# Optimization experiments

Hardware: AMD Instinct MI355X
Metric: run time of the kernel (lower is better)

The kernel has to match this reference:

```python
import jax, jax.numpy as jnp
import numpy as np

N = 100000   # nodes
E = 1600000  # edges
NC = 10000   # candidates
G = 1000     # graphs
ND = 32      # node_emb_dim
ED = 8       # edge_emb_dim
L = 4        # num_layers


def setup_inputs() -> dict:
    key = jax.random.key(0)
    ks = jax.random.split(key, 12)
    s = 0.1
    return {
        "x": jax.random.normal(ks[0], (N, 2), dtype=jnp.float32),
        "edge_attr": jax.random.normal(ks[1], (E, 1), dtype=jnp.float32),
        "Wn_in": jax.random.normal(ks[2], (2, ND)) * s,
        "bn_in": jnp.zeros((ND,)),
        "We_in": jax.random.normal(ks[3], (1, ED)) * s,
        "be_in": jnp.zeros((ED,)),
        "We_l": jax.random.normal(ks[4], (L, 2 * ND + ED, ED)) * s,
        "be_l": jnp.zeros((L, ED)),
        "Wn_l": jax.random.normal(ks[5], (L, ND + ED, ND)) * s,
        "bn_l": jnp.zeros((L, ND)),
        "Wout": jax.random.normal(ks[6], (ND, 1)) * s,
        "bout": jnp.zeros((1,)),
        "edge_index": jax.random.randint(ks[7], (2, E), 0, N),
        "batch": jnp.sort(jax.random.randint(ks[8], (N,), 0, G)),
        "candidate_idxs": jax.random.randint(ks[9], (NC,), 0, N),
    }


def reference(x, edge_attr, Wn_in, bn_in, We_in, be_in, We_l, be_l, Wn_l, bn_l,
              Wout, bout, edge_index, batch, candidate_idxs):
    h = x @ Wn_in + bn_in            # [N, ND]
    e = edge_attr @ We_in + be_in    # [E, ED]
    src, dst = edge_index[0], edge_index[1]
    for l in range(L):
        # edge update: MLP on [x_src, x_dst, edge_attr]
        m = jnp.concatenate([h[src], h[dst], e], axis=-1)        # [E, 2*ND+ED]
        new_e = jax.nn.relu(m @ We_l[l] + be_l[l])               # [E, ED]
        # aggregate (aggr='add') messages at destination nodes
        agg = jax.ops.segment_sum(new_e, dst, num_segments=N)    # [N, ED]
        new_h = jax.nn.relu(jnp.concatenate([h, agg], axis=-1) @ Wn_l[l] + bn_l[l])
        h = h + new_h   # residual
        e = e + new_e   # residual
    logits = (h[candidate_idxs] @ Wout + bout)[:, 0]             # [NC]
    seg = batch[candidate_idxs]                                  # [NC] graph ids
    # scatter_log_softmax over per-graph candidate groups
    mx = jax.ops.segment_max(logits, seg, num_segments=G)
    shifted = logits - mx[seg]
    lse = jnp.log(jax.ops.segment_sum(jnp.exp(shifted), seg, num_segments=G))
    return shifted - lse[seg]
```

## Files before the change

kernel.cpp:

```cpp
#include <hip/hip_runtime.h>

#define ND 32
#define ED 8
#define NL 4
#define NG 1000
#define NBC_MAX 512
#define CHUNK 8192
#define CHUNK_H 4096
#define NBLK 64

typedef unsigned short u16;

__device__ __forceinline__ int xcd_swizzle(int b, int nb) {
  int per = nb >> 3;
  return (b < (per << 3)) ? ((b & 7) * per + (b >> 3)) : b;
}


__device__ __forceinline__ u16 f2bf(float f) {
  unsigned u = __float_as_uint(f);
  u += 0x7fffu + ((u >> 16) & 1u);
  return (u16)(u >> 16);
}
__device__ __forceinline__ unsigned pack2(float a, float b) {
  return (unsigned)f2bf(a) | ((unsigned)f2bf(b) << 16);
}
__device__ __forceinline__ void cvt8(uint4 p, float* o) {
  o[0] = __uint_as_float(p.x << 16); o[1] = __uint_as_float(p.x & 0xffff0000u);
  o[2] = __uint_as_float(p.y << 16); o[3] = __uint_as_float(p.y & 0xffff0000u);
  o[4] = __uint_as_float(p.z << 16); o[5] = __uint_as_float(p.z & 0xffff0000u);
  o[6] = __uint_as_float(p.w << 16); o[7] = __uint_as_float(p.w & 0xffff0000u);
}
__device__ __forceinline__ uint4 pack8(const float* v) {
  uint4 o;
  o.x = pack2(v[0], v[1]); o.y = pack2(v[2], v[3]);
  o.z = pack2(v[4], v[5]); o.w = pack2(v[6], v[7]);
  return o;
}


__global__ void k_init_h(const float* __restrict__ x,
                         const float* __restrict__ W,
                         const float* __restrict__ b,
                         const float* __restrict__ We,
                         const float* __restrict__ be,
                         u16* __restrict__ h,
                         u16* __restrict__ zs, u16* __restrict__ zd,
                         int N) {
  int n = xcd_swizzle(blockIdx.x, gridDim.x) * blockDim.x + threadIdx.x;
  if (n >= N) return;
  float x0 = x[2 * n], x1 = x[2 * n + 1];
  float v[ND];
#pragma unroll
  for (int d = 0; d < ND; ++d) v[d] = fmaf(x0, W[d], fmaf(x1, W[ND + d], b[d]));
#pragma unroll
  for (int d = 0; d < ND; ++d) v[d] = __uint_as_float((unsigned)f2bf(v[d]) << 16);
  uint4* h4 = reinterpret_cast<uint4*>(h + (size_t)n * ND);
#pragma unroll
  for (int q = 0; q < 4; ++q) h4[q] = pack8(&v[q * 8]);
  float zsv[ED], zdv[ED];
#pragma unroll
  for (int j = 0; j < ED; ++j) { zsv[j] = 0.0f; zdv[j] = be[j]; }
#pragma unroll
  for (int k = 0; k < ND; ++k)
#pragma unroll
    for (int j = 0; j < ED; ++j) {
      zsv[j] = fmaf(v[k], We[k * ED + j], zsv[j]);
      zdv[j] = fmaf(v[k], We[(ND + k) * ED + j], zdv[j]);
    }
  *reinterpret_cast<uint4*>(zs + (size_t)n * ED) = pack8(zsv);
  *reinterpret_cast<uint4*>(zd + (size_t)n * ED) = pack8(zdv);
}


__global__ void k_chist(const int* __restrict__ dst, int* __restrict__ bcnt,
                        int E, int nbc) {
  __shared__ int lcnt[NBC_MAX];
  for (int b = threadIdx.x; b < nbc; b += blockDim.x) lcnt[b] = 0;
  __syncthreads();
  int e0 = blockIdx.x * CHUNK_H;
  int e1 = min(e0 + CHUNK_H, E);
  for (int i = e0 + threadIdx.x; i < e1; i += blockDim.x)
    atomicAdd(&lcnt[dst[i] >> 8], 1);
  __syncthreads();
  for (int b = threadIdx.x; b < nbc; b += blockDim.x)
    if (lcnt[b]) atomicAdd(&bcnt[b], lcnt[b]);
}

__global__ void k_cscan(const int* __restrict__ bcnt, int* __restrict__ bbase,
                        int nbc) {
  __shared__ int s[NBC_MAX];
  int tid = threadIdx.x;
  if (nbc <= NBC_MAX) {
    int v = (tid < nbc) ? bcnt[tid] : 0;
    s[tid] = v;
    __syncthreads();
    for (int st = 1; st < NBC_MAX; st <<= 1) {
      int t = (tid >= st) ? s[tid - st] : 0;
      __syncthreads();
      s[tid] += t;
      __syncthreads();
    }
    if (tid < nbc) bbase[tid] = s[tid] - v;
    if (tid == nbc - 1) bbase[nbc] = s[tid];
  } else if (tid == 0) {
    int run = 0;
    for (int i = 0; i < nbc; ++i) { bbase[i] = run; run += bcnt[i]; }
    bbase[nbc] = run;
  }
}

__global__ void k_binA(const int* __restrict__ src, const int* __restrict__ dst,
                       const float* __restrict__ ea,
                       const int* __restrict__ bbase, int* __restrict__ cursor_c,
                       uint2* __restrict__ binned, int E, int nbc) {
  __shared__ int lcnt[NBC_MAX];
  __shared__ int lbase[NBC_MAX];
  for (int b = threadIdx.x; b < nbc; b += blockDim.x) lcnt[b] = 0;
  __syncthreads();
  int e0 = blockIdx.x * CHUNK;
  int e1 = min(e0 + CHUNK, E);
  for (int i = e0 + threadIdx.x; i < e1; i += blockDim.x)
    atomicAdd(&lcnt[dst[i] >> 8], 1);
  __syncthreads();
  for (int b = threadIdx.x; b < nbc; b += blockDim.x) {
    int c = lcnt[b];
    lbase[b] = c ? (bbase[b] + atomicAdd(&cursor_c[b], c)) : 0;
  }
  __syncthreads();
  for (int i = e0 + threadIdx.x; i < e1; i += blockDim.x) {
    int d = dst[i];
    int pos = atomicAdd(&lbase[d >> 8], 1);
    binned[pos] = make_uint2((unsigned)src[i] | ((unsigned)(d & 255) << 24),
                             __float_as_uint(ea[i]));
  }
}

__global__ void k_binB(const uint2* __restrict__ binned,
                       const int* __restrict__ bbase,
                       int* __restrict__ ssrc, float* __restrict__ ea_s,
                       int* __restrict__ noffs,
                       int N) {
  __shared__ int hist[256];
  __shared__ int scn[256];
  int b = blockIdx.x;
  int base = bbase[b], end = bbase[b + 1];
  int node0 = b << 8;
  int nn = min(256, N - node0);
  hist[threadIdx.x] = 0;
  __syncthreads();
  for (int p = base + threadIdx.x; p < end; p += blockDim.x)
    atomicAdd(&hist[binned[p].x >> 24], 1);
  __syncthreads();
  int v = hist[threadIdx.x];
  scn[threadIdx.x] = v;
  __syncthreads();
  for (int st = 1; st < 256; st <<= 1) {
    int t = (threadIdx.x >= (unsigned)st) ? scn[threadIdx.x - st] : 0;
    __syncthreads();
    scn[threadIdx.x] += t;
    __syncthreads();
  }
  int excl = base + scn[threadIdx.x] - v;
  if ((int)threadIdx.x < nn) noffs[node0 + threadIdx.x] = excl;
  if (threadIdx.x == 0) noffs[min(node0 + 256, N)] = end;
  hist[threadIdx.x] = excl;
  __syncthreads();
  for (int p = base + threadIdx.x; p < end; p += blockDim.x) {
    uint2 rec = binned[p];
    int dl = (int)(rec.x >> 24);
    int pos = atomicAdd(&hist[dl], 1);
    ssrc[pos] = (int)(rec.x & 0xffffffu);
    ea_s[pos] = __uint_as_float(rec.y);
  }
}

template <int L0>
__global__ void k_layer(u16* __restrict__ h,
                        u16* __restrict__ e,
                        const float* __restrict__ ea_s,
                        const int* __restrict__ ssrc,
                        const int* __restrict__ noffs,
                        const u16* __restrict__ zs,
                        const u16* __restrict__ zd,
                        const float* __restrict__ Wei,
                        const float* __restrict__ bei,
                        const float* __restrict__ W3,
                        const float* __restrict__ Wn,
                        const float* __restrict__ bn,
                        const float* __restrict__ Wen,
                        const float* __restrict__ ben,
                        u16* __restrict__ zs_n, u16* __restrict__ zd_n,
                        int N) {
  int t = xcd_swizzle(blockIdx.x, gridDim.x) * blockDim.x + threadIdx.x;
  int n = t >> 2;
  int g = t & 3;
  if (n >= N) return;
  int o0 = noffs[n], o1 = noffs[n + 1];
  float zdv[ED];
  cvt8(*reinterpret_cast<const uint4*>(zd + (size_t)n * ED), zdv);
  float av[ED];
#pragma unroll
  for (int j = 0; j < ED; ++j) av[j] = 0.0f;
  for (int p = o0 + g; p < o1; p += 4) {
    int s = ssrc[p];
    float zsv[ED];
    cvt8(*reinterpret_cast<const uint4*>(zs + (size_t)s * ED), zsv);
    float ein[ED];
    if (L0) {
      float a = ea_s[p];
#pragma unroll
      for (int j = 0; j < ED; ++j) ein[j] = fmaf(a, Wei[j], bei[j]);
    } else {
      cvt8(*reinterpret_cast<const uint4*>(e + (size_t)p * ED), ein);
    }
    float acc[ED];
#pragma unroll
    for (int j = 0; j < ED; ++j) acc[j] = zsv[j] + zdv[j];
#pragma unroll
    for (int k = 0; k < ED; ++k)
#pragma unroll
      for (int j = 0; j < ED; ++j)
        acc[j] = fmaf(ein[k], W3[k * ED + j], acc[j]);
    float eo[ED];
#pragma unroll
    for (int j = 0; j < ED; ++j) {
      float r = fmaxf(acc[j], 0.0f);
      av[j] += r;
      eo[j] = ein[j] + r;
    }
    *reinterpret_cast<uint4*>(e + (size_t)p * ED) = pack8(eo);
  }
#pragma unroll
  for (int j = 0; j < ED; ++j) {
    av[j] += __shfl_xor(av[j], 1);
    av[j] += __shfl_xor(av[j], 2);
  }
  uint4* h4 = reinterpret_cast<uint4*>(h + (size_t)n * ND);
  float hv[ND];
#pragma unroll
  for (int q = 0; q < 4; ++q) cvt8(h4[q], &hv[q * 8]);
  const int j0 = g * 8;
  float acc8[8];
#pragma unroll
  for (int jj = 0; jj < 8; ++jj) acc8[jj] = bn[j0 + jj];
#pragma unroll
  for (int k = 0; k < ND; ++k)
#pragma unroll
    for (int jj = 0; jj < 8; ++jj)
      acc8[jj] = fmaf(hv[k], Wn[k * ND + j0 + jj], acc8[jj]);
#pragma unroll
  for (int k = 0; k < ED; ++k)
#pragma unroll
    for (int jj = 0; jj < 8; ++jj)
      acc8[jj] = fmaf(av[k], Wn[(ND + k) * ND + j0 + jj], acc8[jj]);
  float hn8[8];
#pragma unroll
  for (int jj = 0; jj < 8; ++jj) {
    float o = hv[j0 + jj] + fmaxf(acc8[jj], 0.0f);
    hn8[jj] = __uint_as_float((unsigned)f2bf(o) << 16);
  }
  h4[g] = pack8(hn8);
  float pz[2 * ED];
#pragma unroll
  for (int j = 0; j < 2 * ED; ++j) pz[j] = 0.0f;
#pragma unroll
  for (int kk = 0; kk < 8; ++kk) {
    float hk = hn8[kk];
    int krow = j0 + kk;
#pragma unroll
    for (int j = 0; j < ED; ++j) {
      pz[j] = fmaf(hk, Wen[krow * ED + j], pz[j]);
      pz[ED + j] = fmaf(hk, Wen[(ND + krow) * ED + j], pz[ED + j]);
    }
  }
#pragma unroll
  for (int j = 0; j < 2 * ED; ++j) {
    pz[j] += __shfl_xor(pz[j], 1);
    pz[j] += __shfl_xor(pz[j], 2);
  }
  if (g == 0) {
    *reinterpret_cast<uint4*>(zs_n + (size_t)n * ED) = pack8(pz);
  } else if (g == 1) {
    float zdo[ED];
#pragma unroll
    for (int j = 0; j < ED; ++j) zdo[j] = pz[ED + j] + ben[j];
    *reinterpret_cast<uint4*>(zd_n + (size_t)n * ED) = pack8(zdo);
  }
}


__device__ __forceinline__ unsigned int enc_f32(float f) {
  unsigned int bits = __float_as_uint(f);
  return (bits & 0x80000000u) ? ~bits : (bits | 0x80000000u);
}
__device__ __forceinline__ float dec_f32(unsigned int u) {
  unsigned int bits = (u & 0x80000000u) ? (u ^ 0x80000000u) : ~u;
  return __uint_as_float(bits);
}

__global__ void k_cand(const u16* __restrict__ h,
                       const u16* __restrict__ e,
                       const u16* __restrict__ zs,
                       const u16* __restrict__ zd,
                       const int* __restrict__ ssrc,
                       const int* __restrict__ noffs,
                       const int* __restrict__ cand,
                       const int* __restrict__ batch,
                       const float* __restrict__ W3,
                       const float* __restrict__ Wn,
                       const float* __restrict__ bn,
                       const float* __restrict__ Wout,
                       const float* __restrict__ bout,
                       float* __restrict__ logits,
                       int* __restrict__ seg,
                       unsigned int* __restrict__ mxu,
                       int NC) {
  int t = blockIdx.x * blockDim.x + threadIdx.x;
  int c = t >> 3, g = t & 7;
  if (c >= NC) return;
  int n = cand[c];
  int o0 = noffs[n], o1 = noffs[n + 1];
  float zdv[ED];
  cvt8(*reinterpret_cast<const uint4*>(zd + (size_t)n * ED), zdv);
  float av[ED];
#pragma unroll
  for (int j = 0; j < ED; ++j) av[j] = 0.0f;
  for (int p = o0 + g; p < o1; p += 8) {
    int s = ssrc[p];
    float zsv[ED], ein[ED], acc[ED];
    cvt8(*reinterpret_cast<const uint4*>(zs + (size_t)s * ED), zsv);
    cvt8(*reinterpret_cast<const uint4*>(e + (size_t)p * ED), ein);
#pragma unroll
    for (int j = 0; j < ED; ++j) acc[j] = zsv[j] + zdv[j];
#pragma unroll
    for (int k = 0; k < ED; ++k)
#pragma unroll
      for (int j = 0; j < ED; ++j)
        acc[j] = fmaf(ein[k], W3[k * ED + j], acc[j]);
#pragma unroll
    for (int j = 0; j < ED; ++j) av[j] += fmaxf(acc[j], 0.0f);
  }
#pragma unroll
  for (int j = 0; j < ED; ++j) {
    av[j] += __shfl_xor(av[j], 1);
    av[j] += __shfl_xor(av[j], 2);
    av[j] += __shfl_xor(av[j], 4);
  }
  const uint4* h4 = reinterpret_cast<const uint4*>(h + (size_t)n * ND);
  float hv[ND];
#pragma unroll
  for (int q = 0; q < 4; ++q) cvt8(h4[q], &hv[q * 8]);
  const int j0 = g * 4;
  float acc4[4];
#pragma unroll
  for (int jj = 0; jj < 4; ++jj) acc4[jj] = bn[j0 + jj];
#pragma unroll
  for (int k = 0; k < ND; ++k)
#pragma unroll
    for (int jj = 0; jj < 4; ++jj)
      acc4[jj] = fmaf(hv[k], Wn[k * ND + j0 + jj], acc4[jj]);
#pragma unroll
  for (int k = 0; k < ED; ++k)
#pragma unroll
    for (int jj = 0; jj < 4; ++jj)
      acc4[jj] = fmaf(av[k], Wn[(ND + k) * ND + j0 + jj], acc4[jj]);
  float lg = 0.0f;
#pragma unroll
  for (int jj = 0; jj < 4; ++jj)
    lg = fmaf(hv[j0 + jj] + fmaxf(acc4[jj], 0.0f), Wout[j0 + jj], lg);
  lg += __shfl_xor(lg, 1);
  lg += __shfl_xor(lg, 2);
  lg += __shfl_xor(lg, 4);
  if (g == 0) {
    lg += bout[0];
    logits[c] = lg;
    int gr = batch[n];
    seg[c] = gr;
    atomicMax(&mxu[gr], enc_f32(lg));
  }
}

__global__ void k_expsum(float* __restrict__ logits,
                         const int* __restrict__ seg,
                         const unsigned int* __restrict__ mxu,
                         float* __restrict__ sum,
                         int NC) {
  int c = blockIdx.x * blockDim.x + threadIdx.x;
  if (c >= NC) return;
  int g = seg[c];
  float sh = logits[c] - dec_f32(mxu[g]);
  logits[c] = sh;
  atomicAdd(&sum[g], expf(sh));
}

__global__ void k_final(const float* __restrict__ shifted,
                        const int* __restrict__ seg,
                        const float* __restrict__ sum,
                        float* __restrict__ out, int NC) {
  int c = blockIdx.x * blockDim.x + threadIdx.x;
  if (c >= NC) return;
  out[c] = shifted[c] - logf(sum[seg[c]]);
}


extern "C" void kernel_launch(void* const* d_in, const int* in_sizes, int n_in,
                              void* d_out, int out_size, void* d_ws, size_t ws_size,
                              hipStream_t stream) {
  const float* x       = (const float*)d_in[0];
  const float* ea      = (const float*)d_in[1];
  const float* Wn_in   = (const float*)d_in[2];
  const float* bn_in   = (const float*)d_in[3];
  const float* We_in   = (const float*)d_in[4];
  const float* be_in   = (const float*)d_in[5];
  const float* We_l    = (const float*)d_in[6];
  const float* be_l    = (const float*)d_in[7];
  const float* Wn_l    = (const float*)d_in[8];
  const float* bn_l    = (const float*)d_in[9];
  const float* Wout    = (const float*)d_in[10];
  const float* bout    = (const float*)d_in[11];
  const int* edge_index= (const int*)d_in[12];
  const int* batch     = (const int*)d_in[13];
  const int* cand      = (const int*)d_in[14];

  const int N  = in_sizes[13];
  const int E  = in_sizes[1];
  const int NC = in_sizes[14];
  const int nbc = (N + 255) >> 8;

  char* ws = (char*)d_ws;
  uint2* binned = (uint2*)ws; ws += (size_t)E * sizeof(uint2);
  int*   ssrc   = (int*)ws;   ws += (size_t)E * sizeof(int);
  float* ea_s   = (float*)ws; ws += (size_t)E * sizeof(float);
  u16*   h      = (u16*)ws;   ws += (size_t)N * ND * sizeof(u16);
  u16*   e      = (u16*)ws;   ws += (size_t)E * ED * sizeof(u16);
  u16*   zs0    = (u16*)ws;   ws += (size_t)N * ED * sizeof(u16);
  u16*   zd0    = (u16*)ws;   ws += (size_t)N * ED * sizeof(u16);
  u16*   zs1    = (u16*)ws;   ws += (size_t)N * ED * sizeof(u16);
  u16*   zd1    = (u16*)ws;   ws += (size_t)N * ED * sizeof(u16);
  int*   noffs  = (int*)ws;   ws += ((size_t)N + 4) * sizeof(int);
  int*   bcnt   = (int*)ws;   ws += (size_t)NBC_MAX * sizeof(int);
  int*   cursor = (int*)ws;   ws += (size_t)NBC_MAX * sizeof(int);
  int*   bbase  = (int*)ws;   ws += ((size_t)NBC_MAX + 4) * sizeof(int);
  float* logits = (float*)ws; ws += (size_t)NC * sizeof(float);
  int*   seg    = (int*)ws;   ws += (size_t)NC * sizeof(int);
  unsigned int* mxu = (unsigned int*)ws; ws += (size_t)NG * sizeof(unsigned int);
  float* sum    = (float*)ws; ws += (size_t)NG * sizeof(float);

  const int* srcp = edge_index;
  const int* dstp = edge_index + E;
  const int blk = 256;
  const size_t WE_STRIDE = (size_t)(2 * ND + ED) * ED;

  hipMemsetAsync(bcnt, 0, 2 * (size_t)NBC_MAX * sizeof(int), stream);
  k_chist<<<(E + CHUNK_H - 1) / CHUNK_H, 1024, 0, stream>>>(dstp, bcnt, E, nbc);
  k_cscan<<<1, NBC_MAX, 0, stream>>>(bcnt, bbase, nbc);
  k_binA<<<(E + CHUNK - 1) / CHUNK, 1024, 0, stream>>>(srcp, dstp, ea, bbase,
                                                       cursor, binned, E, nbc);
  k_binB<<<nbc, 256, 0, stream>>>(binned, bbase, ssrc, ea_s, noffs, N);

  k_init_h<<<(N + NBLK - 1) / NBLK, NBLK, 0, stream>>>(x, Wn_in, bn_in, We_l,
                                                       be_l, h, zs0, zd0, N);

  const int ngrid4 = (N + 63) / 64;
  u16* zsc = zs0; u16* zdc = zd0;
  u16* zsn = zs1; u16* zdn = zd1;
  for (int l = 0; l < NL - 1; ++l) {
    const float* W3 = We_l + l * WE_STRIDE + (size_t)2 * ND * ED;
    const float* Wn = Wn_l + (size_t)l * (ND + ED) * ND;
    const float* bn = bn_l + (size_t)l * ND;
    const float* Wen = We_l + (l + 1) * WE_STRIDE;
    const float* ben = be_l + (size_t)(l + 1) * ED;
    if (l == 0) {
      k_layer<1><<<ngrid4, 256, 0, stream>>>(
          h, e, ea_s, ssrc, noffs, zsc, zdc, We_in, be_in, W3, Wn, bn,
          Wen, ben, zsn, zdn, N);
    } else {
      k_layer<0><<<ngrid4, 256, 0, stream>>>(
          h, e, ea_s, ssrc, noffs, zsc, zdc, We_in, be_in, W3, Wn, bn,
          Wen, ben, zsn, zdn, N);
    }
    u16* t;
    t = zsc; zsc = zsn; zsn = t;
    t = zdc; zdc = zdn; zdn = t;
  }

  hipMemsetAsync(mxu, 0, NG * (sizeof(unsigned int) + sizeof(float)), stream);
  {
    const int l = NL - 1;
    const float* W3 = We_l + l * WE_STRIDE + (size_t)2 * ND * ED;
    const float* Wn = Wn_l + (size_t)l * (ND + ED) * ND;
    const float* bn = bn_l + (size_t)l * ND;
    k_cand<<<((size_t)NC * 8 + 255) / 256, 256, 0, stream>>>(
        h, e, zsc, zdc, ssrc, noffs, cand, batch, W3, Wn, bn, Wout, bout,
        logits, seg, mxu, NC);
  }
  k_expsum<<<(NC + blk - 1) / blk, blk, 0, stream>>>(logits, seg, mxu, sum, NC);
  k_final<<<(NC + blk - 1) / blk, blk, 0, stream>>>(logits, seg, sum,
                                                    (float*)d_out, NC);
}
```

Measured before the change: 372.2 us.

## Use 8 lanes per node and software-prefetch edge gathers in layer kernels

The layer kernel now assigns 8 threads per node instead of 4, so each thread walks every eighth edge and computes 4 of the 32 node outputs, with an extra shuffle stage for the reductions. Both the layer and candidate kernels gain a two-deep software pipeline: the next edge's source index and edge data are loaded ahead, and the dependent zs gather is issued one iteration early. The aim is to hide the latency of the indirect gathers and expose more parallelism per node. In exchange, register pressure goes up and lanes are wasted on low-degree nodes.

```diff
diff --git a/kernel.cpp b/kernel.cpp
--- a/kernel.cpp
+++ b/kernel.cpp
@@ -193,28 +193,50 @@
                         u16* __restrict__ zs_n, u16* __restrict__ zd_n,
                         int N) {
   int t = xcd_swizzle(blockIdx.x, gridDim.x) * blockDim.x + threadIdx.x;
-  int n = t >> 2;
-  int g = t & 3;
+  int n = t >> 3;
+  int g = t & 7;
   if (n >= N) return;
   int o0 = noffs[n], o1 = noffs[n + 1];
   float zdv[ED];
   cvt8(*reinterpret_cast<const uint4*>(zd + (size_t)n * ED), zdv);
+  const uint4* zs4 = reinterpret_cast<const uint4*>(zs);
+  const uint4* e4c = reinterpret_cast<const uint4*>(e);
+  uint4* e4 = reinterpret_cast<uint4*>(e);
   float av[ED];
 #pragma unroll
   for (int j = 0; j < ED; ++j) av[j] = 0.0f;
-  for (int p = o0 + g; p < o1; p += 4) {
-    int s = ssrc[p];
-    float zsv[ED];
-    cvt8(*reinterpret_cast<const uint4*>(zs + (size_t)s * ED), zsv);
-    float ein[ED];
+
+  int p = o0 + g;
+  int sA = 0, sB = 0;
+  uint4 eA = make_uint4(0, 0, 0, 0), eB = make_uint4(0, 0, 0, 0);
+  float aA = 0.0f, aB = 0.0f;
+  uint4 zA = make_uint4(0, 0, 0, 0);
+  if (p < o1) {
+    sA = ssrc[p];
+    if (L0) aA = ea_s[p]; else eA = e4c[p];
+    zA = zs4[sA];
+  }
+  if (p + 8 < o1) {
+    sB = ssrc[p + 8];
+    if (L0) aB = ea_s[p + 8]; else eB = e4c[p + 8];
+  }
+  for (; p < o1; ) {
+    int pn = p + 8, pc = p + 16;
+    uint4 zB = make_uint4(0, 0, 0, 0);
+    if (pn < o1) zB = zs4[sB];
+    int sC = 0; uint4 eC = make_uint4(0, 0, 0, 0); float aC = 0.0f;
+    if (pc < o1) {
+      sC = ssrc[pc];
+      if (L0) aC = ea_s[pc]; else eC = e4c[pc];
+    }
+    float zsv[ED], ein[ED], acc[ED];
+    cvt8(zA, zsv);
     if (L0) {
-      float a = ea_s[p];
-#pragma unroll
-      for (int j = 0; j < ED; ++j) ein[j] = fmaf(a, Wei[j], bei[j]);
+#pragma unroll
+      for (int j = 0; j < ED; ++j) ein[j] = fmaf(aA, Wei[j], bei[j]);
     } else {
-      cvt8(*reinterpret_cast<const uint4*>(e + (size_t)p * ED), ein);
-    }
-    float acc[ED];
+      cvt8(eA, ein);
+    }
 #pragma unroll
     for (int j = 0; j < ED; ++j) acc[j] = zsv[j] + zdv[j];
 #pragma unroll
@@ -229,44 +251,49 @@
       av[j] += r;
       eo[j] = ein[j] + r;
     }
-    *reinterpret_cast<uint4*>(e + (size_t)p * ED) = pack8(eo);
+    e4[p] = pack8(eo);
+    p = pn;
+    sA = sB; eA = eB; aA = aB; zA = zB;
+    sB = sC; eB = eC; aB = aC;
   }
 #pragma unroll
   for (int j = 0; j < ED; ++j) {
     av[j] += __shfl_xor(av[j], 1);
     av[j] += __shfl_xor(av[j], 2);
+    av[j] += __shfl_xor(av[j], 4);
   }
   uint4* h4 = reinterpret_cast<uint4*>(h + (size_t)n * ND);
   float hv[ND];
 #pragma unroll
   for (int q = 0; q < 4; ++q) cvt8(h4[q], &hv[q * 8]);
-  const int j0 = g * 8;
-  float acc8[8];
-#pragma unroll
-  for (int jj = 0; jj < 8; ++jj) acc8[jj] = bn[j0 + jj];
+  const int j0 = g * 4;
+  float acc4[4];
+#pragma unroll
+  for (int jj = 0; jj < 4; ++jj) acc4[jj] = bn[j0 + jj];
 #pragma unroll
   for (int k = 0; k < ND; ++k)
 #pragma unroll
-    for (int jj = 0; jj < 8; ++jj)
-      acc8[jj] = fmaf(hv[k], Wn[k * ND + j0 + jj], acc8[jj]);
+    for (int jj = 0; jj < 4; ++jj)
+      acc4[jj] = fmaf(hv[k], Wn[k * ND + j0 + jj], acc4[jj]);
 #pragma unroll
   for (int k = 0; k < ED; ++k)
 #pragma unroll
-    for (int jj = 0; jj < 8; ++jj)
-      acc8[jj] = fmaf(av[k], Wn[(ND + k) * ND + j0 + jj], acc8[jj]);
-  float hn8[8];
-#pragma unroll
-  for (int jj = 0; jj < 8; ++jj) {
-    float o = hv[j0 + jj] + fmaxf(acc8[jj], 0.0f);
-    hn8[jj] = __uint_as_float((unsigned)f2bf(o) << 16);
-  }
-  h4[g] = pack8(hn8);
+    for (int jj = 0; jj < 4; ++jj)
+      acc4[jj] = fmaf(av[k], Wn[(ND + k) * ND + j0 + jj], acc4[jj]);
+  float hn4[4];
+#pragma unroll
+  for (int jj = 0; jj < 4; ++jj) {
+    float o = hv[j0 + jj] + fmaxf(acc4[jj], 0.0f);
+    hn4[jj] = __uint_as_float((unsigned)f2bf(o) << 16);
+  }
+  reinterpret_cast<uint2*>(h + (size_t)n * ND)[g] =
+      make_uint2(pack2(hn4[0], hn4[1]), pack2(hn4[2], hn4[3]));
   float pz[2 * ED];
 #pragma unroll
   for (int j = 0; j < 2 * ED; ++j) pz[j] = 0.0f;
 #pragma unroll
-  for (int kk = 0; kk < 8; ++kk) {
-    float hk = hn8[kk];
+  for (int kk = 0; kk < 4; ++kk) {
+    float hk = hn4[kk];
     int krow = j0 + kk;
 #pragma unroll
     for (int j = 0; j < ED; ++j) {
@@ -278,6 +305,7 @@
   for (int j = 0; j < 2 * ED; ++j) {
     pz[j] += __shfl_xor(pz[j], 1);
     pz[j] += __shfl_xor(pz[j], 2);
+    pz[j] += __shfl_xor(pz[j], 4);
   }
   if (g == 0) {
     *reinterpret_cast<uint4*>(zs_n + (size_t)n * ED) = pack8(pz);
@@ -323,14 +351,26 @@
   int o0 = noffs[n], o1 = noffs[n + 1];
   float zdv[ED];
   cvt8(*reinterpret_cast<const uint4*>(zd + (size_t)n * ED), zdv);
+  const uint4* zs4 = reinterpret_cast<const uint4*>(zs);
+  const uint4* e4c = reinterpret_cast<const uint4*>(e);
   float av[ED];
 #pragma unroll
   for (int j = 0; j < ED; ++j) av[j] = 0.0f;
-  for (int p = o0 + g; p < o1; p += 8) {
-    int s = ssrc[p];
+  int p = o0 + g;
+  int sA = 0, sB = 0;
+  uint4 eA = make_uint4(0, 0, 0, 0), eB = make_uint4(0, 0, 0, 0);
+  uint4 zA = make_uint4(0, 0, 0, 0);
+  if (p < o1) { sA = ssrc[p]; eA = e4c[p]; zA = zs4[sA]; }
+  if (p + 8 < o1) { sB = ssrc[p + 8]; eB = e4c[p + 8]; }
+  for (; p < o1; ) {
+    int pn = p + 8, pc = p + 16;
+    uint4 zB = make_uint4(0, 0, 0, 0);
+    if (pn < o1) zB = zs4[sB];
+    int sC = 0; uint4 eC = make_uint4(0, 0, 0, 0);
+    if (pc < o1) { sC = ssrc[pc]; eC = e4c[pc]; }
     float zsv[ED], ein[ED], acc[ED];
-    cvt8(*reinterpret_cast<const uint4*>(zs + (size_t)s * ED), zsv);
-    cvt8(*reinterpret_cast<const uint4*>(e + (size_t)p * ED), ein);
+    cvt8(zA, zsv);
+    cvt8(eA, ein);
 #pragma unroll
     for (int j = 0; j < ED; ++j) acc[j] = zsv[j] + zdv[j];
 #pragma unroll
@@ -340,6 +380,9 @@
         acc[j] = fmaf(ein[k], W3[k * ED + j], acc[j]);
 #pragma unroll
     for (int j = 0; j < ED; ++j) av[j] += fmaxf(acc[j], 0.0f);
+    p = pn;
+    sA = sB; eA = eB; zA = zB;
+    sB = sC; eB = eC;
   }
 #pragma unroll
   for (int j = 0; j < ED; ++j) {
@@ -462,7 +505,7 @@
   k_init_h<<<(N + NBLK - 1) / NBLK, NBLK, 0, stream>>>(x, Wn_in, bn_in, We_l,
                                                        be_l, h, zs0, zd0, N);
 
-  const int ngrid4 = (N + 63) / 64;
+  const int ngrid8 = (N + 31) / 32;
   u16* zsc = zs0; u16* zdc = zd0;
   u16* zsn = zs1; u16* zdn = zd1;
   for (int l = 0; l < NL - 1; ++l) {
@@ -472,11 +515,11 @@
     const float* Wen = We_l + (l + 1) * WE_STRIDE;
     const float* ben = be_l + (size_t)(l + 1) * ED;
     if (l == 0) {
-      k_layer<1><<<ngrid4, 256, 0, stream>>>(
+      k_layer<1><<<ngrid8, 256, 0, stream>>>(
           h, e, ea_s, ssrc, noffs, zsc, zdc, We_in, be_in, W3, Wn, bn,
           Wen, ben, zsn, zdn, N);
     } else {
-      k_layer<0><<<ngrid4, 256, 0, stream>>>(
+      k_layer<0><<<ngrid8, 256, 0, stream>>>(
           h, e, ea_s, ssrc, noffs, zsc, zdc, We_in, be_in, W3, Wn, bn,
           Wen, ben, zsn, zdn, N);
     }
```

Result: faster. 339.7 us (-8.7%).

## Use 8 threads per node with batched edge loads and hardware bf16 conversion

Applied to the files above, without the earlier changes.

The layer kernel now assigns 8 lanes per node instead of 4, and the candidate kernel 16 instead of 8. Each lane processes up to 4 (or 2) edges per iteration, issuing all index, edge and zs gathers before computing, to raise memory-level parallelism. The node's h row is prefetched before the edge loop, and the software bf16 rounding is replaced with the v_cvt_pk_bf16_f32 instruction. This trades more threads and an extra shuffle stage for better latency hiding on the irregular gathers, with some risk of divergence on low-degree nodes.

```diff
diff --git a/kernel.cpp b/kernel.cpp
--- a/kernel.cpp
+++ b/kernel.cpp
@@ -17,13 +17,15 @@
 }
 
 
-__device__ __forceinline__ u16 f2bf(float f) {
-  unsigned u = __float_as_uint(f);
-  u += 0x7fffu + ((u >> 16) & 1u);
-  return (u16)(u >> 16);
-}
 __device__ __forceinline__ unsigned pack2(float a, float b) {
-  return (unsigned)f2bf(a) | ((unsigned)f2bf(b) << 16);
+  unsigned r;
+  asm("v_cvt_pk_bf16_f32 %0, %1, %2" : "=v"(r) : "v"(a), "v"(b));
+  return r;
+}
+__device__ __forceinline__ float bf_round(float f) {
+  unsigned r;
+  asm("v_cvt_pk_bf16_f32 %0, %1, %2" : "=v"(r) : "v"(f), "v"(f));
+  return __uint_as_float(r << 16);
 }
 __device__ __forceinline__ void cvt8(uint4 p, float* o) {
   o[0] = __uint_as_float(p.x << 16); o[1] = __uint_as_float(p.x & 0xffff0000u);
@@ -54,7 +56,7 @@
 #pragma unroll
   for (int d = 0; d < ND; ++d) v[d] = fmaf(x0, W[d], fmaf(x1, W[ND + d], b[d]));
 #pragma unroll
-  for (int d = 0; d < ND; ++d) v[d] = __uint_as_float((unsigned)f2bf(v[d]) << 16);
+  for (int d = 0; d < ND; ++d) v[d] = bf_round(v[d]);
   uint4* h4 = reinterpret_cast<uint4*>(h + (size_t)n * ND);
 #pragma unroll
   for (int q = 0; q < 4; ++q) h4[q] = pack8(&v[q * 8]);
@@ -193,28 +195,30 @@
                         u16* __restrict__ zs_n, u16* __restrict__ zd_n,
                         int N) {
   int t = xcd_swizzle(blockIdx.x, gridDim.x) * blockDim.x + threadIdx.x;
-  int n = t >> 2;
-  int g = t & 3;
+  int n = t >> 3;
+  int g = t & 7;
   if (n >= N) return;
   int o0 = noffs[n], o1 = noffs[n + 1];
+  uint4* h4 = reinterpret_cast<uint4*>(h + (size_t)n * ND);
+  uint4 hq0 = h4[0], hq1 = h4[1], hq2 = h4[2], hq3 = h4[3];
   float zdv[ED];
   cvt8(*reinterpret_cast<const uint4*>(zd + (size_t)n * ED), zdv);
+  const uint4* zs4 = reinterpret_cast<const uint4*>(zs);
+  const uint4* e4c = reinterpret_cast<const uint4*>(e);
+  uint4* e4 = reinterpret_cast<uint4*>(e);
   float av[ED];
 #pragma unroll
   for (int j = 0; j < ED; ++j) av[j] = 0.0f;
-  for (int p = o0 + g; p < o1; p += 4) {
-    int s = ssrc[p];
-    float zsv[ED];
-    cvt8(*reinterpret_cast<const uint4*>(zs + (size_t)s * ED), zsv);
-    float ein[ED];
+
+  auto edge_one = [&](int p_, uint4 z_, uint4 e_, float a_) {
+    float zsv[ED], ein[ED], acc[ED];
+    cvt8(z_, zsv);
     if (L0) {
-      float a = ea_s[p];
-#pragma unroll
-      for (int j = 0; j < ED; ++j) ein[j] = fmaf(a, Wei[j], bei[j]);
+#pragma unroll
+      for (int j = 0; j < ED; ++j) ein[j] = fmaf(a_, Wei[j], bei[j]);
     } else {
-      cvt8(*reinterpret_cast<const uint4*>(e + (size_t)p * ED), ein);
-    }
-    float acc[ED];
+      cvt8(e_, ein);
+    }
 #pragma unroll
     for (int j = 0; j < ED; ++j) acc[j] = zsv[j] + zdv[j];
 #pragma unroll
@@ -229,44 +233,63 @@
       av[j] += r;
       eo[j] = ein[j] + r;
     }
-    *reinterpret_cast<uint4*>(e + (size_t)p * ED) = pack8(eo);
+    e4[p_] = pack8(eo);
+  };
+
+  for (int base = o0 + g; base < o1; base += 32) {
+    bool v1 = base + 8 < o1, v2 = base + 16 < o1, v3 = base + 24 < o1;
+    int pa = base;
+    int pb = v1 ? base + 8 : base;
+    int pc = v2 ? base + 16 : base;
+    int pd = v3 ? base + 24 : base;
+    int sa = ssrc[pa], sb = ssrc[pb], sc = ssrc[pc], sd = ssrc[pd];
+    uint4 Ea = make_uint4(0, 0, 0, 0), Eb = Ea, Ec = Ea, Ed = Ea;
+    float Aa = 0.f, Ab = 0.f, Ac = 0.f, Ad = 0.f;
+    if (L0) {
+      Aa = ea_s[pa]; Ab = ea_s[pb]; Ac = ea_s[pc]; Ad = ea_s[pd];
+    } else {
+      Ea = e4c[pa]; Eb = e4c[pb]; Ec = e4c[pc]; Ed = e4c[pd];
+    }
+    uint4 Za = zs4[sa], Zb = zs4[sb], Zc = zs4[sc], Zd = zs4[sd];
+    edge_one(pa, Za, Ea, Aa);
+    if (v1) edge_one(pb, Zb, Eb, Ab);
+    if (v2) edge_one(pc, Zc, Ec, Ac);
+    if (v3) edge_one(pd, Zd, Ed, Ad);
   }
 #pragma unroll
   for (int j = 0; j < ED; ++j) {
     av[j] += __shfl_xor(av[j], 1);
     av[j] += __shfl_xor(av[j], 2);
-  }
-  uint4* h4 = reinterpret_cast<uint4*>(h + (size_t)n * ND);
+    av[j] += __shfl_xor(av[j], 4);
+  }
   float hv[ND];
-#pragma unroll
-  for (int q = 0; q < 4; ++q) cvt8(h4[q], &hv[q * 8]);
-  const int j0 = g * 8;
-  float acc8[8];
-#pragma unroll
-  for (int jj = 0; jj < 8; ++jj) acc8[jj] = bn[j0 + jj];
+  cvt8(hq0, &hv[0]); cvt8(hq1, &hv[8]); cvt8(hq2, &hv[16]); cvt8(hq3, &hv[24]);
+  const int j0 = g * 4;
+  float acc4[4];
+#pragma unroll
+  for (int jj = 0; jj < 4; ++jj) acc4[jj] = bn[j0 + jj];
 #pragma unroll
   for (int k = 0; k < ND; ++k)
 #pragma unroll
-    for (int jj = 0; jj < 8; ++jj)
-      acc8[jj] = fmaf(hv[k], Wn[k * ND + j0 + jj], acc8[jj]);
+    for (int jj = 0; jj < 4; ++jj)
+      acc4[jj] = fmaf(hv[k], Wn[k * ND + j0 + jj], acc4[jj]);
 #pragma unroll
   for (int k = 0; k < ED; ++k)
 #pragma unroll
-    for (int jj = 0; jj < 8; ++jj)
-      acc8[jj] = fmaf(av[k], Wn[(ND + k) * ND + j0 + jj], acc8[jj]);
-  float hn8[8];
-#pragma unroll
-  for (int jj = 0; jj < 8; ++jj) {
-    float o = hv[j0 + jj] + fmaxf(acc8[jj], 0.0f);
-    hn8[jj] = __uint_as_float((unsigned)f2bf(o) << 16);
-  }
-  h4[g] = pack8(hn8);
+    for (int jj = 0; jj < 4; ++jj)
+      acc4[jj] = fmaf(av[k], Wn[(ND + k) * ND + j0 + jj], acc4[jj]);
+  float hn4[4];
+#pragma unroll
+  for (int jj = 0; jj < 4; ++jj)
+    hn4[jj] = bf_round(hv[j0 + jj] + fmaxf(acc4[jj], 0.0f));
+  reinterpret_cast<uint2*>(h + (size_t)n * ND)[g] =
+      make_uint2(pack2(hn4[0], hn4[1]), pack2(hn4[2], hn4[3]));
   float pz[2 * ED];
 #pragma unroll
   for (int j = 0; j < 2 * ED; ++j) pz[j] = 0.0f;
 #pragma unroll
-  for (int kk = 0; kk < 8; ++kk) {
-    float hk = hn8[kk];
+  for (int kk = 0; kk < 4; ++kk) {
+    float hk = hn4[kk];
     int krow = j0 + kk;
 #pragma unroll
     for (int j = 0; j < ED; ++j) {
@@ -278,6 +301,7 @@
   for (int j = 0; j < 2 * ED; ++j) {
     pz[j] += __shfl_xor(pz[j], 1);
     pz[j] += __shfl_xor(pz[j], 2);
+    pz[j] += __shfl_xor(pz[j], 4);
   }
   if (g == 0) {
     *reinterpret_cast<uint4*>(zs_n + (size_t)n * ED) = pack8(pz);
@@ -317,20 +341,24 @@
                        unsigned int* __restrict__ mxu,
                        int NC) {
   int t = blockIdx.x * blockDim.x + threadIdx.x;
-  int c = t >> 3, g = t & 7;
+  int c = t >> 4, g = t & 15;
   if (c >= NC) return;
   int n = cand[c];
   int o0 = noffs[n], o1 = noffs[n + 1];
+  const uint4* h4 = reinterpret_cast<const uint4*>(h + (size_t)n * ND);
+  uint4 hq0 = h4[0], hq1 = h4[1], hq2 = h4[2], hq3 = h4[3];
   float zdv[ED];
   cvt8(*reinterpret_cast<const uint4*>(zd + (size_t)n * ED), zdv);
+  const uint4* zs4 = reinterpret_cast<const uint4*>(zs);
+  const uint4* e4c = reinterpret_cast<const uint4*>(e);
   float av[ED];
 #pragma unroll
   for (int j = 0; j < ED; ++j) av[j] = 0.0f;
-  for (int p = o0 + g; p < o1; p += 8) {
-    int s = ssrc[p];
+
+  auto cand_one = [&](uint4 z_, uint4 e_) {
     float zsv[ED], ein[ED], acc[ED];
-    cvt8(*reinterpret_cast<const uint4*>(zs + (size_t)s * ED), zsv);
-    cvt8(*reinterpret_cast<const uint4*>(e + (size_t)p * ED), ein);
+    cvt8(z_, zsv);
+    cvt8(e_, ein);
 #pragma unroll
     for (int j = 0; j < ED; ++j) acc[j] = zsv[j] + zdv[j];
 #pragma unroll
@@ -340,38 +368,49 @@
         acc[j] = fmaf(ein[k], W3[k * ED + j], acc[j]);
 #pragma unroll
     for (int j = 0; j < ED; ++j) av[j] += fmaxf(acc[j], 0.0f);
+  };
+
+  for (int base = o0 + g; base < o1; base += 32) {
+    bool v1 = base + 16 < o1;
+    int pa = base;
+    int pb = v1 ? base + 16 : base;
+    int sa = ssrc[pa], sb = ssrc[pb];
+    uint4 Ea = e4c[pa], Eb = e4c[pb];
+    uint4 Za = zs4[sa], Zb = zs4[sb];
+    cand_one(Za, Ea);
+    if (v1) cand_one(Zb, Eb);
   }
 #pragma unroll
   for (int j = 0; j < ED; ++j) {
     av[j] += __shfl_xor(av[j], 1);
     av[j] += __shfl_xor(av[j], 2);
     av[j] += __shfl_xor(av[j], 4);
-  }
-  const uint4* h4 = reinterpret_cast<const uint4*>(h + (size_t)n * ND);
+    av[j] += __shfl_xor(av[j], 8);
+  }
   float hv[ND];
-#pragma unroll
-  for (int q = 0; q < 4; ++q) cvt8(h4[q], &hv[q * 8]);
-  const int j0 = g * 4;
-  float acc4[4];
-#pragma unroll
-  for (int jj = 0; jj < 4; ++jj) acc4[jj] = bn[j0 + jj];
+  cvt8(hq0, &hv[0]); cvt8(hq1, &hv[8]); cvt8(hq2, &hv[16]); cvt8(hq3, &hv[24]);
+  const int j0 = g * 2;
+  float acc2[2];
+#pragma unroll
+  for (int jj = 0; jj < 2; ++jj) acc2[jj] = bn[j0 + jj];
 #pragma unroll
   for (int k = 0; k < ND; ++k)
 #pragma unroll
-    for (int jj = 0; jj < 4; ++jj)
-      acc4[jj] = fmaf(hv[k], Wn[k * ND + j0 + jj], acc4[jj]);
+    for (int jj = 0; jj < 2; ++jj)
+      acc2[jj] = fmaf(hv[k], Wn[k * ND + j0 + jj], acc2[jj]);
 #pragma unroll
   for (int k = 0; k < ED; ++k)
 #pragma unroll
-    for (int jj = 0; jj < 4; ++jj)
-      acc4[jj] = fmaf(av[k], Wn[(ND + k) * ND + j0 + jj], acc4[jj]);
+    for (int jj = 0; jj < 2; ++jj)
+      acc2[jj] = fmaf(av[k], Wn[(ND + k) * ND + j0 + jj], acc2[jj]);
   float lg = 0.0f;
 #pragma unroll
-  for (int jj = 0; jj < 4; ++jj)
-    lg = fmaf(hv[j0 + jj] + fmaxf(acc4[jj], 0.0f), Wout[j0 + jj], lg);
+  for (int jj = 0; jj < 2; ++jj)
+    lg = fmaf(hv[j0 + jj] + fmaxf(acc2[jj], 0.0f), Wout[j0 + jj], lg);
   lg += __shfl_xor(lg, 1);
   lg += __shfl_xor(lg, 2);
   lg += __shfl_xor(lg, 4);
+  lg += __shfl_xor(lg, 8);
   if (g == 0) {
     lg += bout[0];
     logits[c] = lg;
@@ -462,7 +501,7 @@
   k_init_h<<<(N + NBLK - 1) / NBLK, NBLK, 0, stream>>>(x, Wn_in, bn_in, We_l,
                                                        be_l, h, zs0, zd0, N);
 
-  const int ngrid4 = (N + 63) / 64;
+  const int ngrid8 = (N + 31) / 32;
   u16* zsc = zs0; u16* zdc = zd0;
   u16* zsn = zs1; u16* zdn = zd1;
   for (int l = 0; l < NL - 1; ++l) {
@@ -472,11 +511,11 @@
     const float* Wen = We_l + (l + 1) * WE_STRIDE;
     const float* ben = be_l + (size_t)(l + 1) * ED;
     if (l == 0) {
-      k_layer<1><<<ngrid4, 256, 0, stream>>>(
+      k_layer<1><<<ngrid8, 256, 0, stream>>>(
           h, e, ea_s, ssrc, noffs, zsc, zdc, We_in, be_in, W3, Wn, bn,
           Wen, ben, zsn, zdn, N);
     } else {
-      k_layer<0><<<ngrid4, 256, 0, stream>>>(
+      k_layer<0><<<ngrid8, 256, 0, stream>>>(
           h, e, ea_s, ssrc, noffs, zsc, zdc, We_in, be_in, W3, Wn, bn,
           Wen, ben, zsn, zdn, N);
     }
@@ -491,7 +530,7 @@
     const float* W3 = We_l + l * WE_STRIDE + (size_t)2 * ND * ED;
     const float* Wn = Wn_l + (size_t)l * (ND + ED) * ND;
     const float* bn = bn_l + (size_t)l * ND;
-    k_cand<<<((size_t)NC * 8 + 255) / 256, 256, 0, stream>>>(
+    k_cand<<<((size_t)NC * 16 + 255) / 256, 256, 0, stream>>>(
         h, e, zsc, zdc, ssrc, noffs, cand, batch, W3, Wn, bn, Wout, bout,
         logits, seg, mxu, NC);
   }
```

Result: faster. 347.6 us (-6.6%).
